# Kernel optimization log

Hardware: AMD Instinct MI355X
Metric: run time of the kernel (lower is better)

Reference implementation:

```python
import jax, jax.numpy as jnp
import numpy as np

BETA = 0.9      # LIF leak
THRESH = 1.0    # snntorch Leaky default threshold
SLOPE = 25.0    # fast_sigmoid surrogate slope

@jax.custom_vjp
def spike(x):
    # Heaviside forward, fast_sigmoid surrogate backward
    return (x > 0).astype(x.dtype)

def _spike_fwd(x):
    return spike(x), x

def _spike_bwd(x, g):
    return (g / (SLOPE * jnp.abs(x) + 1.0) ** 2,)

spike.defvjp(_spike_fwd, _spike_bwd)


def setup_inputs() -> dict:
    key = jax.random.key(0)
    k0, k1, k2, k3, k4 = jax.random.split(key, 5)
    B, T, I, H, C = 256, 100, 512, 1024, 8
    x = jax.random.normal(k0, (B, T, I), dtype=jnp.float32)
    s1 = 1.0 / np.sqrt(I)
    s2 = 1.0 / np.sqrt(H)
    W1 = jax.random.uniform(k1, (H, I), jnp.float32, -s1, s1)
    b1 = jax.random.uniform(k2, (H,), jnp.float32, -s1, s1)
    W2 = jax.random.uniform(k3, (C, H), jnp.float32, -s2, s2)
    b2 = jax.random.uniform(k4, (C,), jnp.float32, -s2, s2)
    return {"x": x, "W1": W1, "b1": b1, "W2": W2, "b2": b2}


def reference(x, W1, b1, W2, b2):
    # x: [B, T, I]
    B, T, I = x.shape
    H = W1.shape[0]
    # fc1 for all timesteps as one big GEMM (same math as per-step loop).
    cur = jnp.einsum('bti,hi->tbh', x, W1) + b1  # [T, B, H]

    def step(mem, c):
        # snntorch Leaky (reset_mechanism='subtract'):
        reset = spike(mem - THRESH)
        mem_new = BETA * mem + c - reset * THRESH
        spk = spike(mem_new - THRESH)
        return mem_new, spk

    mem0 = jnp.zeros((B, H), dtype=x.dtype)
    _, spk_rec = jax.lax.scan(step, mem0, cur)  # spk_rec: [T, B, H]

    # sum_t (spk_t @ W2.T + b2) == (sum_t spk_t) @ W2.T + T*b2
    spk_sum = spk_rec.sum(axis=0)  # [B, H]
    logits = spk_sum @ W2.T + T * b2  # [B, C]
    return logits
```

## Files before the change

### kernel.cpp

```cpp
#include <hip/hip_runtime.h>


#define B_   256
#define T_   100
#define I_   512
#define H_   1024
#define C_   8
#define M_   (B_ * T_)
#define KS_  1024
#define SC   64.0f
#define ISC  (1.0f / 4096.0f)

typedef _Float16 half8 __attribute__((ext_vector_type(8)));
typedef float floatx16 __attribute__((ext_vector_type(16)));

__device__ __forceinline__ void ld_g2l(const _Float16* g, _Float16* l) {
    __builtin_amdgcn_global_load_lds(
        (const __attribute__((address_space(1))) void*)g,
        (__attribute__((address_space(3))) void*)l, 16, 0, 0);
}

__global__ void __launch_bounds__(256)
split_all(const float* __restrict__ x, const float* __restrict__ W1,
          const float* __restrict__ b2, _Float16* __restrict__ Asp,
          float* __restrict__ out) {
    int g = blockIdx.x * 256 + threadIdx.x;
    if (g < B_ * C_) out[g] = 100.0f * b2[g & (C_ - 1)];
    int row = g >> 6;
    int i0 = (g & 63) * 8;
    const float* src = (row < M_) ? (x + (size_t)row * I_ + i0)
                                  : (W1 + (size_t)(row - M_) * I_ + i0);
    float4 v0 = *(const float4*)(src);
    float4 v1 = *(const float4*)(src + 4);
    float vv[8] = {v0.x, v0.y, v0.z, v0.w, v1.x, v1.y, v1.z, v1.w};
    half8 hi, lo;
#pragma unroll
    for (int j = 0; j < 8; ++j) {
        float s = vv[j] * SC;
        _Float16 h = (_Float16)s;
        hi[j] = h;
        lo[j] = (_Float16)(s - (float)h);
    }
    _Float16* r = Asp + (size_t)row * KS_ + i0;
    *(half8*)(r) = hi;
    *(half8*)(r + 512) = lo;
}

#define MFMA32(A, Bv, Cacc) \
    Cacc = __builtin_amdgcn_mfma_f32_32x32x16_f16(A, Bv, Cacc, 0, 0, 0)

#define STAGE(dd, koff) do {                                         \
    _Float16* lb = &sm.buf[0][0] + (dd) * 12288;                     \
    ld_g2l(ga0 + (koff), lb + w * 512);                              \
    ld_g2l(ga1 + (koff), lb + 2048 + w * 512);                       \
    ld_g2l(gb00 + (koff), lb + 4096 + w * 1024);                     \
    ld_g2l(gb01 + (koff), lb + 4096 + w * 1024 + 512);               \
    ld_g2l(gb10 + (koff), lb + 8192 + w * 1024);                     \
    ld_g2l(gb11 + (koff), lb + 8192 + w * 1024 + 512);               \
} while (0)

#define COMPUTE(dd) do {                                             \
    const _Float16* bb = &sm.buf[0][0] + (dd) * 12288;               \
    half8 ah[2], al[2], bh[4], bl[4];                                \
    _Pragma("unroll")                                                \
    for (int f = 0; f < 2; ++f) {                                    \
        ah[f] = *(const half8*)(bb + ra + f * 512);                  \
        al[f] = *(const half8*)(bb + 2048 + ra + f * 512);           \
    }                                                                \
    _Pragma("unroll")                                                \
    for (int f = 0; f < 4; ++f) {                                    \
        bh[f] = *(const half8*)(bb + 4096 + rb + f * 512);           \
        bl[f] = *(const half8*)(bb + 8192 + rb + f * 512);           \
    }                                                                \
    _Pragma("unroll")                                                \
    for (int fm = 0; fm < 2; ++fm) {                                 \
        _Pragma("unroll")                                            \
        for (int fn = 0; fn < 4; ++fn) {                             \
            MFMA32(ah[fm], bh[fn], acc[fm][fn]);                     \
            MFMA32(ah[fm], bl[fn], acc[fm][fn]);                     \
            MFMA32(al[fm], bh[fn], acc[fm][fn]);                     \
        }                                                            \
    }                                                                \
} while (0)

__global__ void __launch_bounds__(256, 2)
snn_mfma(const _Float16* __restrict__ Asp, const _Float16* __restrict__ Wsp,
         const float* __restrict__ b1, const float* __restrict__ W2,
         float* __restrict__ logits) {
    __shared__ union {
        __align__(16) _Float16 buf[2][12288];
        float Cs[64 * 256];
    } sm;
    const int tid = threadIdx.x;
    const int lane = tid & 63;
    const int w = tid >> 6;

    const int xcd = blockIdx.x & 7;
    const int jj = blockIdx.x >> 3;
    const int b  = xcd * 32 + (jj >> 2);
    const int n0 = (jj & 3) * 256;

    const int wm = (w >> 1) * 64;
    const int wn = (w & 1) * 128;
    const int l31 = lane & 31;
    const int q2 = lane >> 5;

    const int rl = lane >> 1;
    const int cl8 = (lane & 1) * 8;
    const _Float16* ga0 = Asp + (size_t)(b * T_ + w * 32 + rl) * KS_ + cl8;
    const _Float16* ga1 = ga0 + 512;
    const _Float16* gb00 = Wsp + (size_t)(n0 + w * 64 + rl) * KS_ + cl8;
    const _Float16* gb01 = gb00 + 32 * KS_;
    const _Float16* gb10 = gb00 + 512;
    const _Float16* gb11 = gb01 + 512;

    const int ra = (wm + l31) * 16 + q2 * 8;
    const int rb = (wn + l31) * 16 + q2 * 8;

    floatx16 acc[2][4];
#pragma unroll
    for (int i = 0; i < 2; ++i)
#pragma unroll
        for (int j = 0; j < 4; ++j)
#pragma unroll
            for (int e = 0; e < 16; ++e) acc[i][j][e] = 0.f;

    STAGE(0, 0);
#pragma unroll 2
    for (int c = 0; c < 31; ++c) {
        const int d = c & 1;
        STAGE(d ^ 1, (c + 1) * 16);
        asm volatile("s_waitcnt vmcnt(6)" ::: "memory");
        __builtin_amdgcn_s_barrier();
        COMPUTE(d);
        __builtin_amdgcn_s_barrier();
        asm volatile("" ::: "memory");
    }
    asm volatile("s_waitcnt vmcnt(0)" ::: "memory");
    __builtin_amdgcn_s_barrier();
    COMPUTE(1);
    __syncthreads();

    float b1c[4];
#pragma unroll
    for (int fn = 0; fn < 4; ++fn) b1c[fn] = b1[n0 + wn + fn * 32 + l31];

    float mem = 0.f, ss = 0.f;

    if (w < 2) {
#pragma unroll
        for (int fm = 0; fm < 2; ++fm)
#pragma unroll
            for (int r = 0; r < 16; ++r) {
                const int row = fm * 32 + (r & 3) + 8 * (r >> 2) + 4 * q2;
                float* dst = &sm.Cs[row * 256 + wn + l31];
#pragma unroll
                for (int fn = 0; fn < 4; ++fn)
                    dst[fn * 32] = acc[fm][fn][r] * ISC + b1c[fn];
            }
    }
    __syncthreads();
#pragma unroll 8
    for (int t = 0; t < 64; ++t) {
        float cv = sm.Cs[t * 256 + tid];
        float reset = (mem > 1.0f) ? 1.0f : 0.0f;
        mem = 0.9f * mem + cv - reset;
        ss += (mem > 1.0f) ? 1.0f : 0.0f;
    }
    __syncthreads();
    if (w >= 2) {
#pragma unroll
        for (int fm = 0; fm < 2; ++fm)
#pragma unroll
            for (int r = 0; r < 16; ++r) {
                const int row = fm * 32 + (r & 3) + 8 * (r >> 2) + 4 * q2;
                float* dst = &sm.Cs[row * 256 + wn + l31];
#pragma unroll
                for (int fn = 0; fn < 4; ++fn)
                    dst[fn * 32] = acc[fm][fn][r] * ISC + b1c[fn];
            }
    }
    __syncthreads();
#pragma unroll 6
    for (int t = 0; t < 36; ++t) {
        float cv = sm.Cs[t * 256 + tid];
        float reset = (mem > 1.0f) ? 1.0f : 0.0f;
        mem = 0.9f * mem + cv - reset;
        ss += (mem > 1.0f) ? 1.0f : 0.0f;
    }
#pragma unroll
    for (int cc = 0; cc < C_; ++cc) {
        float v = ss * W2[cc * H_ + n0 + tid];
#pragma unroll
        for (int off = 32; off; off >>= 1) v += __shfl_down(v, off, 64);
        if (lane == 0) atomicAdd(&logits[b * C_ + cc], v);
    }
}

extern "C" void kernel_launch(void* const* d_in, const int* in_sizes, int n_in,
                              void* d_out, int out_size, void* d_ws, size_t ws_size,
                              hipStream_t stream) {
    const float* x  = (const float*)d_in[0];
    const float* W1 = (const float*)d_in[1];
    const float* b1 = (const float*)d_in[2];
    const float* W2 = (const float*)d_in[3];
    const float* b2 = (const float*)d_in[4];
    float* out = (float*)d_out;

    char* ws = (char*)d_ws;
    _Float16* Asp = (_Float16*)ws;
    _Float16* Wsp = (_Float16*)(ws + (size_t)M_ * KS_ * 2);

    hipLaunchKernelGGL(split_all, dim3((M_ + H_) * 64 / 256), dim3(256), 0, stream,
                       x, W1, b2, Asp, out);
    hipLaunchKernelGGL(snn_mfma, dim3(B_ * 4), dim3(256), 0, stream,
                       Asp, Wsp, b1, W2, out);
}
```

Before: 216.4 us.

## Swizzle LDS tiles, halve epilogue scratch, and raise occupancy to three blocks

Applies an XOR swizzle to both the global-to-LDS load lane mapping and the fragment read offsets, so MFMA operand reads hit fewer LDS bank conflicts. The epilogue now stages the accumulator in four 32-row chunks instead of two 64-row chunks, which halves the shared scratch so the union shrinks to the 48KB double buffer. Launch bounds are raised to 3 blocks per SM for higher occupancy. This adds more barriers in the epilogue and may force register spilling under the tighter register budget.

```diff
diff --git a/kernel.cpp b/kernel.cpp
--- a/kernel.cpp
+++ b/kernel.cpp
@@ -83,13 +83,13 @@
     }                                                                \
 } while (0)
 
-__global__ void __launch_bounds__(256, 2)
+__global__ void __launch_bounds__(256, 3)
 snn_mfma(const _Float16* __restrict__ Asp, const _Float16* __restrict__ Wsp,
          const float* __restrict__ b1, const float* __restrict__ W2,
          float* __restrict__ logits) {
     __shared__ union {
         __align__(16) _Float16 buf[2][12288];
-        float Cs[64 * 256];
+        float Cs[32 * 256];
     } sm;
     const int tid = threadIdx.x;
     const int lane = tid & 63;
@@ -105,8 +105,9 @@
     const int l31 = lane & 31;
     const int q2 = lane >> 5;
 
-    const int rl = lane >> 1;
-    const int cl8 = (lane & 1) * 8;
+    const int lp = lane ^ ((lane >> 3) & 7);
+    const int rl = lp >> 1;
+    const int cl8 = (lp & 1) * 8;
     const _Float16* ga0 = Asp + (size_t)(b * T_ + w * 32 + rl) * KS_ + cl8;
     const _Float16* ga1 = ga0 + 512;
     const _Float16* gb00 = Wsp + (size_t)(n0 + w * 64 + rl) * KS_ + cl8;
@@ -114,8 +115,9 @@
     const _Float16* gb10 = gb00 + 512;
     const _Float16* gb11 = gb01 + 512;
 
-    const int ra = (wm + l31) * 16 + q2 * 8;
-    const int rb = (wn + l31) * 16 + q2 * 8;
+    const int swz = ((l31 >> 2) & 7) << 3;
+    const int ra = (((wm + l31) * 16) + q2 * 8) ^ swz;
+    const int rb = (((wn + l31) * 16) + q2 * 8) ^ swz;
 
     floatx16 acc[2][4];
 #pragma unroll
@@ -147,47 +149,31 @@
 
     float mem = 0.f, ss = 0.f;
 
-    if (w < 2) {
-#pragma unroll
-        for (int fm = 0; fm < 2; ++fm)
+#pragma unroll
+    for (int p = 0; p < 4; ++p) {
+        const int fm = p & 1;
+        if ((w >> 1) == (p >> 1)) {
 #pragma unroll
             for (int r = 0; r < 16; ++r) {
-                const int row = fm * 32 + (r & 3) + 8 * (r >> 2) + 4 * q2;
+                const int row = (r & 3) + 8 * (r >> 2) + 4 * q2;
                 float* dst = &sm.Cs[row * 256 + wn + l31];
 #pragma unroll
                 for (int fn = 0; fn < 4; ++fn)
                     dst[fn * 32] = acc[fm][fn][r] * ISC + b1c[fn];
             }
-    }
-    __syncthreads();
+        }
+        __syncthreads();
+        const int nt = (p == 3) ? 4 : 32;
 #pragma unroll 8
-    for (int t = 0; t < 64; ++t) {
-        float cv = sm.Cs[t * 256 + tid];
-        float reset = (mem > 1.0f) ? 1.0f : 0.0f;
-        mem = 0.9f * mem + cv - reset;
-        ss += (mem > 1.0f) ? 1.0f : 0.0f;
-    }
-    __syncthreads();
-    if (w >= 2) {
-#pragma unroll
-        for (int fm = 0; fm < 2; ++fm)
-#pragma unroll
-            for (int r = 0; r < 16; ++r) {
-                const int row = fm * 32 + (r & 3) + 8 * (r >> 2) + 4 * q2;
-                float* dst = &sm.Cs[row * 256 + wn + l31];
-#pragma unroll
-                for (int fn = 0; fn < 4; ++fn)
-                    dst[fn * 32] = acc[fm][fn][r] * ISC + b1c[fn];
-            }
-    }
-    __syncthreads();
-#pragma unroll 6
-    for (int t = 0; t < 36; ++t) {
-        float cv = sm.Cs[t * 256 + tid];
-        float reset = (mem > 1.0f) ? 1.0f : 0.0f;
-        mem = 0.9f * mem + cv - reset;
-        ss += (mem > 1.0f) ? 1.0f : 0.0f;
-    }
+        for (int t = 0; t < nt; ++t) {
+            float cv = sm.Cs[t * 256 + tid];
+            float reset = (mem > 1.0f) ? 1.0f : 0.0f;
+            mem = 0.9f * mem + cv - reset;
+            ss += (mem > 1.0f) ? 1.0f : 0.0f;
+        }
+        __syncthreads();
+    }
+
 #pragma unroll
     for (int cc = 0; cc < C_; ++cc) {
         float v = ss * W2[cc * H_ + n0 + tid];
```

New measurement: 363.0 us. 1.68x slower.
